# Optimization experiments

Hardware: AMD Instinct MI355X
Metric: run time of the kernel (lower is better)

The kernel has to match this reference:

```python
import jax, jax.numpy as jnp
import numpy as np


def _segsum(x):
    """Stable segment sum: exp(segsum(A)) is 1-semiseparable. x: (..., T) -> (..., T, T)."""
    T = x.shape[-1]
    xx = jnp.broadcast_to(x[..., None], (*x.shape, T))
    xx = jnp.where(jnp.tril(jnp.ones((T, T), bool), -1), xx, 0.0)
    s = jnp.cumsum(xx, axis=-2)
    return jnp.where(jnp.tril(jnp.ones((T, T), bool), 0), s, -jnp.inf)


def setup_inputs() -> dict:
    key = jax.random.key(0)
    ks = jax.random.split(key, 6)
    b, T, h, p, n = 2, 1024, 32, 64, 128
    x = jax.random.normal(ks[0], (b, T, h, p), jnp.float32)
    # negative decay rates, as produced by -exp(A_log)*softplus(dt) in Mamba2
    A = -jax.random.uniform(ks[1], (b, T, h), jnp.float32, minval=0.01, maxval=0.5)
    B = jax.random.normal(ks[2], (b, T, h, n), jnp.float32)
    C = jax.random.normal(ks[3], (b, T, h, n), jnp.float32)
    # retrieval similarity mask (lower-triangular, like segment_and_cosine_similarity output)
    L_mask = jax.random.uniform(ks[4], (b, h, T, T), jnp.float32) * jnp.tril(jnp.ones((T, T), jnp.float32))
    mask_scaling_factor = jnp.float32(0.5)
    return {"x": x, "A": A, "B": B, "C": C, "L_mask": L_mask,
            "mask_scaling_factor": mask_scaling_factor, "chunk_size": 64}


def reference(x, A, B, C, L_mask, mask_scaling_factor, chunk_size):
    b, T, h, p = x.shape
    n = B.shape[-1]
    l = chunk_size
    k = T // l
    # chunk: b (c l) ... -> b c l ...
    xr = x.reshape(b, k, l, h, p)
    Br = B.reshape(b, k, l, h, n)
    Cr = C.reshape(b, k, l, h, n)
    Ar = jnp.transpose(A.reshape(b, k, l, h), (0, 3, 1, 2))  # b h c l
    A_cs = jnp.cumsum(Ar, axis=-1)                            # b h c l
    L = jnp.exp(_segsum(Ar))                                  # b h c l l
    # decompose_diagonal_and_lower_tri(L_mask, chunk_size)
    r = L_mask.reshape(b, h, k, l, k, l)
    didx = np.arange(k)
    L_mask_diag = jnp.moveaxis(r[:, :, didx, :, didx, :], 0, 2)          # b h k l l
    row_idx, col_idx = np.tril_indices(k, -1)                             # strict lower block pairs
    lower_tri = jnp.moveaxis(r[:, :, row_idx, :, col_idx, :], 0, 2)       # b h P l l
    L = L + mask_scaling_factor * L_mask_diag
    # diagonal (intra-chunk) blocks
    Y_diag = jnp.einsum('bclhn,bcshn,bhcls,bcshp->bclhp', Cr, Br, L, xr)
    # retrieval off-diagonal blocks, scatter-added back per destination chunk
    Y_tmp = jnp.einsum('bclhn,bcshn,bhcls,bcshp->bclhp',
                       Cr[:, row_idx], Br[:, col_idx],
                       mask_scaling_factor * lower_tri, xr[:, col_idx])   # b P l h p
    Y_retr = jnp.moveaxis(
        jax.ops.segment_sum(jnp.moveaxis(Y_tmp, 1, 0), jnp.asarray(row_idx), num_segments=k),
        0, 1)                                                             # b k l h p
    # inter-chunk state passing
    decay_states = jnp.exp(A_cs[..., -1:] - A_cs)                         # b h c l
    states = jnp.einsum('bclhn,bhcl,bclhp->bchpn', Br, decay_states, xr)  # b c h p n
    states = jnp.concatenate([jnp.zeros_like(states[:, :1]), states], axis=1)
    decay_chunk = jnp.exp(_segsum(jnp.pad(A_cs[..., -1], ((0, 0), (0, 0), (1, 0)))))  # b h (k+1) (k+1)
    new_states = jnp.einsum('bhzc,bchpn->bzhpn', decay_chunk, states)
    states_in, final_state = new_states[:, :-1], new_states[:, -1]
    Y_off = jnp.einsum('bclhn,bchpn,bhcl->bclhp', Cr, states_in, jnp.exp(A_cs))
    Y = (Y_diag + Y_off + Y_retr).reshape(b, T, h, p)
    return Y, final_state
```

## Files before the change

kernel.cpp:

```cpp
#include <hip/hip_runtime.h>

#define T_ 1024
#define H_ 32
#define P_ 64
#define N_ 128
#define L_ 64

typedef float f32x4 __attribute__((ext_vector_type(4)));
typedef short short8 __attribute__((ext_vector_type(8)));
typedef short short4v __attribute__((ext_vector_type(4)));

static __device__ __forceinline__ unsigned short f2bf(float f) {
  unsigned int u = __float_as_uint(f);
  u += 0x7fffu + ((u >> 16) & 1u);
  return (unsigned short)(u >> 16);
}
static __device__ __forceinline__ float bf2f(short s) {
  return __uint_as_float(((unsigned int)(unsigned short)s) << 16);
}

__global__ __launch_bounds__(1024) void cuma_kernel(const float* __restrict__ A,
                                                    float* __restrict__ cumA) {
  const int bh = blockIdx.x;
  const int b = bh >> 5, h = bh & 31;
  const int t = threadIdx.x;
  __shared__ float s[1024];
  s[t] = A[(b * T_ + t) * H_ + h];
  __syncthreads();
  for (int off = 1; off < 1024; off <<= 1) {
    float v = (t >= off) ? s[t - off] : 0.0f;
    __syncthreads();
    s[t] += v;
    __syncthreads();
  }
  cumA[bh * T_ + t] = s[t];
}

__global__ __launch_bounds__(256) void prep_kernel(
    const float* __restrict__ x, const float* __restrict__ Bm,
    const float* __restrict__ Cm, short* __restrict__ Bbf,
    short* __restrict__ BT, short* __restrict__ Cbf,
    short* __restrict__ xT) {
  const int bh = blockIdx.x;
  const int tb = blockIdx.y;
  const int b = bh >> 5, h = bh & 31;
  const int tid = threadIdx.x;
  __shared__ short Bt[128][72];
  __shared__ short Xt[64][72];

#pragma unroll
  for (int i = 0; i < 8; ++i) {
    const int idx = tid + 256 * i;
    const int row = idx >> 5, n4 = idx & 31;
    const float4 v = *(const float4*)(Bm + ((size_t)(b * T_ + tb * 64 + row) * H_ + h) * N_ + n4 * 4);
    short4v o;
    o.x = (short)f2bf(v.x); o.y = (short)f2bf(v.y);
    o.z = (short)f2bf(v.z); o.w = (short)f2bf(v.w);
    *(short4v*)(Bbf + ((size_t)bh * T_ + tb * 64 + row) * N_ + n4 * 4) = o;
    Bt[n4 * 4 + 0][row] = o.x; Bt[n4 * 4 + 1][row] = o.y;
    Bt[n4 * 4 + 2][row] = o.z; Bt[n4 * 4 + 3][row] = o.w;
  }
#pragma unroll
  for (int i = 0; i < 8; ++i) {
    const int idx = tid + 256 * i;
    const int row = idx >> 5, n4 = idx & 31;
    const float4 v = *(const float4*)(Cm + ((size_t)(b * T_ + tb * 64 + row) * H_ + h) * N_ + n4 * 4);
    short4v o;
    o.x = (short)f2bf(v.x); o.y = (short)f2bf(v.y);
    o.z = (short)f2bf(v.z); o.w = (short)f2bf(v.w);
    *(short4v*)(Cbf + ((size_t)bh * T_ + tb * 64 + row) * N_ + n4 * 4) = o;
  }
#pragma unroll
  for (int i = 0; i < 4; ++i) {
    const int idx = tid + 256 * i;
    const int row = idx >> 4, p4 = idx & 15;
    const float4 v = *(const float4*)(x + ((size_t)(b * T_ + tb * 64 + row) * H_ + h) * P_ + p4 * 4);
    Xt[p4 * 4 + 0][row] = (short)f2bf(v.x);
    Xt[p4 * 4 + 1][row] = (short)f2bf(v.y);
    Xt[p4 * 4 + 2][row] = (short)f2bf(v.z);
    Xt[p4 * 4 + 3][row] = (short)f2bf(v.w);
  }
  __syncthreads();
#pragma unroll
  for (int i = 0; i < 4; ++i) {
    const int idx = tid + 256 * i;
    const int n = idx >> 3, t8 = idx & 7;
    const short4v a = *(const short4v*)&Bt[n][t8 * 8];
    const short4v c = *(const short4v*)&Bt[n][t8 * 8 + 4];
    short8 o;
    o[0] = a.x; o[1] = a.y; o[2] = a.z; o[3] = a.w;
    o[4] = c.x; o[5] = c.y; o[6] = c.z; o[7] = c.w;
    *(short8*)(BT + ((size_t)bh * N_ + n) * T_ + tb * 64 + t8 * 8) = o;
  }
#pragma unroll
  for (int i = 0; i < 2; ++i) {
    const int idx = tid + 256 * i;
    const int p = idx >> 3, t8 = idx & 7;
    const short4v a = *(const short4v*)&Xt[p][t8 * 8];
    const short4v c = *(const short4v*)&Xt[p][t8 * 8 + 4];
    short8 o;
    o[0] = a.x; o[1] = a.y; o[2] = a.z; o[3] = a.w;
    o[4] = c.x; o[5] = c.y; o[6] = c.z; o[7] = c.w;
    *(short8*)(xT + ((size_t)bh * P_ + p) * T_ + tb * 64 + t8 * 8) = o;
  }
}

__global__ __launch_bounds__(256, 2) void attn_kernel(
    const short* __restrict__ xT, const short* __restrict__ Bbf,
    const short* __restrict__ Cbf, const float* __restrict__ mask,
    const float* __restrict__ msf_p, const float* __restrict__ cumA,
    float* __restrict__ Y) {
  const int blk = blockIdx.x;
  const int qc = 15 - (blk >> 6);
  const int bh = blk & 63;
  const int b = bh >> 5, h = bh & 31;
  const float msf = msf_p[0];
  const int tid = threadIdx.x;
  const int w = tid >> 6;
  const int lane = tid & 63;
  const int q = lane >> 4, c = lane & 15;

  __shared__ short Ps[4][16][72];

  short8 cf[4];
  {
    const short* Cg = Cbf + ((size_t)bh * T_ + qc * L_ + 16 * w + c) * N_ + 8 * q;
#pragma unroll
    for (int kt = 0; kt < 4; ++kt) cf[kt] = *(const short8*)(Cg + kt * 32);
  }
  float ca_i[4];
#pragma unroll
  for (int r = 0; r < 4; ++r)
    ca_i[r] = cumA[bh * T_ + qc * L_ + 16 * w + 4 * q + r];

  f32x4 yacc[4];
#pragma unroll
  for (int pt = 0; pt < 4; ++pt) yacc[pt] = (f32x4){0.f, 0.f, 0.f, 0.f};

  const float* mrow0 = mask + ((size_t)bh * T_ + (size_t)(qc * L_ + 16 * w + 4 * q)) * T_ + c;
  const short* Bg0 = Bbf + (size_t)bh * T_ * N_ + 8 * q;
  const short* xg0 = xT + (size_t)bh * P_ * T_ + 8 * q;

  float mvA[16], mvB[16], ckA[4], ckB[4];
#pragma unroll
  for (int tj = 0; tj < 4; ++tj)
#pragma unroll
    for (int r = 0; r < 4; ++r)
      mvA[tj * 4 + r] = __builtin_nontemporal_load(mrow0 + (size_t)r * T_ + 16 * tj);
#pragma unroll
  for (int tj = 0; tj < 4; ++tj) ckA[tj] = cumA[bh * T_ + 16 * tj + c];

#define ATTN_STEP(KC, MVI, CKI, MVO, CKO)                                      \
  {                                                                            \
    const int kc_ = (KC);                                                      \
    const int kcn_ = (kc_ + 1 <= qc) ? (kc_ + 1) : qc;                         \
    short8 bfr[16];                                                            \
    const short* Bg = Bg0 + (size_t)kc_ * L_ * N_;                             \
    _Pragma("unroll") for (int kt = 0; kt < 4; ++kt)                           \
        _Pragma("unroll") for (int tj = 0; tj < 4; ++tj)                       \
            bfr[kt * 4 + tj] =                                                 \
        *(const short8*)(Bg + (size_t)(16 * tj + c) * N_ + kt * 32);           \
    short8 xfr[8];                                                             \
    const short* xg = xg0 + kc_ * L_;                                          \
    _Pragma("unroll") for (int kt2 = 0; kt2 < 2; ++kt2)                        \
        _Pragma("unroll") for (int pt = 0; pt < 4; ++pt)                       \
            xfr[kt2 * 4 + pt] =                                                \
        *(const short8*)(xg + (size_t)(16 * pt + c) * T_ + kt2 * 32);          \
    const float* mb = mrow0 + (size_t)kcn_ * L_;                               \
    _Pragma("unroll") for (int tj = 0; tj < 4; ++tj)                           \
        _Pragma("unroll") for (int r = 0; r < 4; ++r)                          \
            MVO[tj * 4 + r] =                                                  \
        __builtin_nontemporal_load(mb + (size_t)r * T_ + 16 * tj);             \
    _Pragma("unroll") for (int tj = 0; tj < 4; ++tj)                           \
        CKO[tj] = cumA[bh * T_ + kcn_ * L_ + 16 * tj + c];                     \
    f32x4 sacc[4];                                                             \
    _Pragma("unroll") for (int tj = 0; tj < 4; ++tj)                           \
        sacc[tj] = (f32x4){0.f, 0.f, 0.f, 0.f};                                \
    _Pragma("unroll") for (int kt = 0; kt < 4; ++kt)                           \
        _Pragma("unroll") for (int tj = 0; tj < 4; ++tj)                       \
            sacc[tj] = __builtin_amdgcn_mfma_f32_16x16x32_bf16(                \
        cf[kt], bfr[kt * 4 + tj], sacc[tj], 0, 0, 0);                          \
    const bool diag = (kc_ == qc);                                             \
    _Pragma("unroll") for (int tj = 0; tj < 4; ++tj) {                         \
      const int j_l = 16 * tj + c;                                             \
      _Pragma("unroll") for (int r = 0; r < 4; ++r) {                          \
        const int i_l = 16 * w + 4 * q + r;                                    \
        float wgt = __expf(ca_i[r] - CKI[tj]) + msf * MVI[tj * 4 + r];         \
        if (diag && j_l > i_l) wgt = 0.0f;                                     \
        Ps[w][4 * q + r][j_l] = (short)f2bf(sacc[tj][r] * wgt);                \
      }                                                                        \
    }                                                                          \
    _Pragma("unroll") for (int kt2 = 0; kt2 < 2; ++kt2) {                      \
      const short8 pf = *(const short8*)&Ps[w][c][kt2 * 32 + 8 * q];           \
      _Pragma("unroll") for (int pt = 0; pt < 4; ++pt)                         \
          yacc[pt] = __builtin_amdgcn_mfma_f32_16x16x32_bf16(                  \
          pf, xfr[kt2 * 4 + pt], yacc[pt], 0, 0, 0);                           \
    }                                                                          \
  }

  int kc = 0;
  for (; kc + 1 <= qc; kc += 2) {
    ATTN_STEP(kc, mvA, ckA, mvB, ckB)
    ATTN_STEP(kc + 1, mvB, ckB, mvA, ckA)
  }
  if (kc <= qc) {
    ATTN_STEP(kc, mvA, ckA, mvB, ckB)
  }
#undef ATTN_STEP

  float* Yg = Y + ((size_t)(b * T_ + qc * L_ + 16 * w + 4 * q) * H_ + h) * P_;
#pragma unroll
  for (int pt = 0; pt < 4; ++pt)
#pragma unroll
    for (int r = 0; r < 4; ++r)
      __builtin_nontemporal_store(yacc[pt][r], Yg + (size_t)r * (H_ * P_) + 16 * pt + c);
}

__global__ __launch_bounds__(256) void zero_fs(float* __restrict__ fs) {
  const int i = blockIdx.x * 256 + threadIdx.x;
  ((float4*)fs)[i] = make_float4(0.f, 0.f, 0.f, 0.f);
}

__global__ __launch_bounds__(256) void state_kernel(
    const short* __restrict__ xT, const short* __restrict__ BT,
    const float* __restrict__ cumA, float* __restrict__ out) {
  const int bh = blockIdx.x;
  const int tq = blockIdx.y;
  const int tid = threadIdx.x;
  const int w = tid >> 6;
  const int lane = tid & 63;
  const int q = lane >> 4, c = lane & 15;

  __shared__ float wsh[256];
  {
    const float cend = cumA[bh * T_ + (T_ - 1)];
    wsh[tid] = __expf(cend - cumA[bh * T_ + tq * 256 + tid]);
  }
  __syncthreads();

  f32x4 acc[8];
#pragma unroll
  for (int nt = 0; nt < 8; ++nt) acc[nt] = (f32x4){0.f, 0.f, 0.f, 0.f};

#pragma unroll
  for (int ktl = 0; ktl < 8; ++ktl) {
    const int t0 = ktl * 32;
    const int tg = tq * 256 + t0;
    const short8 xv = *(const short8*)(xT + ((size_t)bh * P_ + 16 * w + c) * T_ + tg + 8 * q);
    const float4 w0 = *(const float4*)&wsh[t0 + 8 * q];
    const float4 w1 = *(const float4*)&wsh[t0 + 8 * q + 4];
    short8 af;
    af[0] = (short)f2bf(bf2f(xv[0]) * w0.x); af[1] = (short)f2bf(bf2f(xv[1]) * w0.y);
    af[2] = (short)f2bf(bf2f(xv[2]) * w0.z); af[3] = (short)f2bf(bf2f(xv[3]) * w0.w);
    af[4] = (short)f2bf(bf2f(xv[4]) * w1.x); af[5] = (short)f2bf(bf2f(xv[5]) * w1.y);
    af[6] = (short)f2bf(bf2f(xv[6]) * w1.z); af[7] = (short)f2bf(bf2f(xv[7]) * w1.w);
#pragma unroll
    for (int nt = 0; nt < 8; ++nt) {
      const short8 bf = *(const short8*)(BT + ((size_t)bh * N_ + 16 * nt + c) * T_ + tg + 8 * q);
      acc[nt] = __builtin_amdgcn_mfma_f32_16x16x32_bf16(af, bf, acc[nt], 0, 0, 0);
    }
  }

  float* o = out + (size_t)bh * P_ * N_;
#pragma unroll
  for (int nt = 0; nt < 8; ++nt)
#pragma unroll
    for (int r = 0; r < 4; ++r)
      atomicAdd(&o[(size_t)(16 * w + 4 * q + r) * N_ + 16 * nt + c], acc[nt][r]);
}

extern "C" void kernel_launch(void* const* d_in, const int* in_sizes, int n_in,
                              void* d_out, int out_size, void* d_ws, size_t ws_size,
                              hipStream_t stream) {
  const float* x    = (const float*)d_in[0];
  const float* A    = (const float*)d_in[1];
  const float* Bm   = (const float*)d_in[2];
  const float* Cm   = (const float*)d_in[3];
  const float* mask = (const float*)d_in[4];
  const float* msf  = (const float*)d_in[5];
  float* Y  = (float*)d_out;
  float* fs = (float*)d_out + (size_t)2 * T_ * H_ * P_;

  char* ws = (char*)d_ws;
  float* cumA = (float*)ws;
  size_t off = 1 << 18;
  short* Bbf = (short*)(ws + off); off += (size_t)64 * T_ * N_ * 2;
  short* BT  = (short*)(ws + off); off += (size_t)64 * T_ * N_ * 2;
  short* Cbf = (short*)(ws + off); off += (size_t)64 * T_ * N_ * 2;
  short* xT  = (short*)(ws + off);

  cuma_kernel<<<64, 1024, 0, stream>>>(A, cumA);
  prep_kernel<<<dim3(64, 16), 256, 0, stream>>>(x, Bm, Cm, Bbf, BT, Cbf, xT);
  attn_kernel<<<1024, 256, 0, stream>>>(xT, Bbf, Cbf, mask, msf, cumA, Y);
  zero_fs<<<512, 256, 0, stream>>>(fs);
  state_kernel<<<dim3(64, 4), 256, 0, stream>>>(xT, BT, cumA, fs);
}
```

Before: 506.0 us.

## Pair complementary query chunks per block and use packed bf16 converts with exp2

```diff
diff --git a/kernel.cpp b/kernel.cpp
--- a/kernel.cpp
+++ b/kernel.cpp
@@ -9,14 +9,27 @@
 typedef float f32x4 __attribute__((ext_vector_type(4)));
 typedef short short8 __attribute__((ext_vector_type(8)));
 typedef short short4v __attribute__((ext_vector_type(4)));
-
-static __device__ __forceinline__ unsigned short f2bf(float f) {
-  unsigned int u = __float_as_uint(f);
-  u += 0x7fffu + ((u >> 16) & 1u);
-  return (unsigned short)(u >> 16);
-}
+typedef unsigned int uint2v __attribute__((ext_vector_type(2)));
+typedef unsigned int uint4v __attribute__((ext_vector_type(4)));
+
+#define LOG2E 1.4426950408889634f
+
 static __device__ __forceinline__ float bf2f(short s) {
   return __uint_as_float(((unsigned int)(unsigned short)s) << 16);
+}
+
+static __device__ __forceinline__ unsigned cvt_pk_bf16(float lo, float hi) {
+  unsigned r;
+  asm("v_cvt_pk_bf16_f32 %0, %1, %2" : "=v"(r) : "v"(lo), "v"(hi));
+  return r;
+}
+
+static __device__ __forceinline__ float fexp2(float x) {
+#if __has_builtin(__builtin_amdgcn_exp2f)
+  return __builtin_amdgcn_exp2f(x);
+#else
+  return __expf(x * 0.6931471805599453f);
+#endif
 }
 
 __global__ __launch_bounds__(1024) void cuma_kernel(const float* __restrict__ A,
@@ -33,7 +46,7 @@
     s[t] += v;
     __syncthreads();
   }
-  cumA[bh * T_ + t] = s[t];
+  cumA[bh * T_ + t] = s[t] * LOG2E;
 }
 
 __global__ __launch_bounds__(256) void prep_kernel(
@@ -53,32 +66,32 @@
     const int idx = tid + 256 * i;
     const int row = idx >> 5, n4 = idx & 31;
     const float4 v = *(const float4*)(Bm + ((size_t)(b * T_ + tb * 64 + row) * H_ + h) * N_ + n4 * 4);
-    short4v o;
-    o.x = (short)f2bf(v.x); o.y = (short)f2bf(v.y);
-    o.z = (short)f2bf(v.z); o.w = (short)f2bf(v.w);
-    *(short4v*)(Bbf + ((size_t)bh * T_ + tb * 64 + row) * N_ + n4 * 4) = o;
-    Bt[n4 * 4 + 0][row] = o.x; Bt[n4 * 4 + 1][row] = o.y;
-    Bt[n4 * 4 + 2][row] = o.z; Bt[n4 * 4 + 3][row] = o.w;
+    const unsigned p0 = cvt_pk_bf16(v.x, v.y);
+    const unsigned p1 = cvt_pk_bf16(v.z, v.w);
+    uint2v o; o.x = p0; o.y = p1;
+    *(uint2v*)(Bbf + ((size_t)bh * T_ + tb * 64 + row) * N_ + n4 * 4) = o;
+    Bt[n4 * 4 + 0][row] = (short)p0; Bt[n4 * 4 + 1][row] = (short)(p0 >> 16);
+    Bt[n4 * 4 + 2][row] = (short)p1; Bt[n4 * 4 + 3][row] = (short)(p1 >> 16);
   }
 #pragma unroll
   for (int i = 0; i < 8; ++i) {
     const int idx = tid + 256 * i;
     const int row = idx >> 5, n4 = idx & 31;
     const float4 v = *(const float4*)(Cm + ((size_t)(b * T_ + tb * 64 + row) * H_ + h) * N_ + n4 * 4);
-    short4v o;
-    o.x = (short)f2bf(v.x); o.y = (short)f2bf(v.y);
-    o.z = (short)f2bf(v.z); o.w = (short)f2bf(v.w);
-    *(short4v*)(Cbf + ((size_t)bh * T_ + tb * 64 + row) * N_ + n4 * 4) = o;
+    uint2v o; o.x = cvt_pk_bf16(v.x, v.y); o.y = cvt_pk_bf16(v.z, v.w);
+    *(uint2v*)(Cbf + ((size_t)bh * T_ + tb * 64 + row) * N_ + n4 * 4) = o;
   }
 #pragma unroll
   for (int i = 0; i < 4; ++i) {
     const int idx = tid + 256 * i;
     const int row = idx >> 4, p4 = idx & 15;
     const float4 v = *(const float4*)(x + ((size_t)(b * T_ + tb * 64 + row) * H_ + h) * P_ + p4 * 4);
-    Xt[p4 * 4 + 0][row] = (short)f2bf(v.x);
-    Xt[p4 * 4 + 1][row] = (short)f2bf(v.y);
-    Xt[p4 * 4 + 2][row] = (short)f2bf(v.z);
-    Xt[p4 * 4 + 3][row] = (short)f2bf(v.w);
+    const unsigned p0 = cvt_pk_bf16(v.x, v.y);
+    const unsigned p1 = cvt_pk_bf16(v.z, v.w);
+    Xt[p4 * 4 + 0][row] = (short)p0;
+    Xt[p4 * 4 + 1][row] = (short)(p0 >> 16);
+    Xt[p4 * 4 + 2][row] = (short)p1;
+    Xt[p4 * 4 + 3][row] = (short)(p1 >> 16);
   }
   __syncthreads();
 #pragma unroll
@@ -111,8 +124,8 @@
     const float* __restrict__ msf_p, const float* __restrict__ cumA,
     float* __restrict__ Y) {
   const int blk = blockIdx.x;
-  const int qc = 15 - (blk >> 6);
   const int bh = blk & 63;
+  const int jj = blk >> 6;
   const int b = bh >> 5, h = bh & 31;
   const float msf = msf_p[0];
   const int tid = threadIdx.x;
@@ -122,33 +135,38 @@
 
   __shared__ short Ps[4][16][72];
 
-  short8 cf[4];
-  {
-    const short* Cg = Cbf + ((size_t)bh * T_ + qc * L_ + 16 * w + c) * N_ + 8 * q;
-#pragma unroll
-    for (int kt = 0; kt < 4; ++kt) cf[kt] = *(const short8*)(Cg + kt * 32);
-  }
-  float ca_i[4];
-#pragma unroll
-  for (int r = 0; r < 4; ++r)
-    ca_i[r] = cumA[bh * T_ + qc * L_ + 16 * w + 4 * q + r];
-
-  f32x4 yacc[4];
-#pragma unroll
-  for (int pt = 0; pt < 4; ++pt) yacc[pt] = (f32x4){0.f, 0.f, 0.f, 0.f};
-
-  const float* mrow0 = mask + ((size_t)bh * T_ + (size_t)(qc * L_ + 16 * w + 4 * q)) * T_ + c;
   const short* Bg0 = Bbf + (size_t)bh * T_ * N_ + 8 * q;
   const short* xg0 = xT + (size_t)bh * P_ * T_ + 8 * q;
 
-  float mvA[16], mvB[16], ckA[4], ckB[4];
-#pragma unroll
-  for (int tj = 0; tj < 4; ++tj)
+#pragma unroll 1
+  for (int pass = 0; pass < 2; ++pass) {
+    const int qc = pass ? jj : (15 - jj);
+
+    short8 cf[4];
+    {
+      const short* Cg = Cbf + ((size_t)bh * T_ + qc * L_ + 16 * w + c) * N_ + 8 * q;
+#pragma unroll
+      for (int kt = 0; kt < 4; ++kt) cf[kt] = *(const short8*)(Cg + kt * 32);
+    }
+    float ca_i[4];
 #pragma unroll
     for (int r = 0; r < 4; ++r)
-      mvA[tj * 4 + r] = __builtin_nontemporal_load(mrow0 + (size_t)r * T_ + 16 * tj);
-#pragma unroll
-  for (int tj = 0; tj < 4; ++tj) ckA[tj] = cumA[bh * T_ + 16 * tj + c];
+      ca_i[r] = cumA[bh * T_ + qc * L_ + 16 * w + 4 * q + r];
+
+    f32x4 yacc[4];
+#pragma unroll
+    for (int pt = 0; pt < 4; ++pt) yacc[pt] = (f32x4){0.f, 0.f, 0.f, 0.f};
+
+    const float* mrow0 = mask + ((size_t)bh * T_ + (size_t)(qc * L_ + 16 * w + 4 * q)) * T_ + c;
+
+    float mvA[16], mvB[16], ckA[4], ckB[4];
+#pragma unroll
+    for (int tj = 0; tj < 4; ++tj)
+#pragma unroll
+      for (int r = 0; r < 4; ++r)
+        mvA[tj * 4 + r] = __builtin_nontemporal_load(mrow0 + (size_t)r * T_ + 16 * tj);
+#pragma unroll
+    for (int tj = 0; tj < 4; ++tj) ckA[tj] = cumA[bh * T_ + 16 * tj + c];
 
 #define ATTN_STEP(KC, MVI, CKI, MVO, CKO)                                      \
   {                                                                            \
@@ -183,12 +201,19 @@
     const bool diag = (kc_ == qc);                                             \
     _Pragma("unroll") for (int tj = 0; tj < 4; ++tj) {                         \
       const int j_l = 16 * tj + c;                                             \
+      float fv[4];                                                             \
       _Pragma("unroll") for (int r = 0; r < 4; ++r) {                          \
         const int i_l = 16 * w + 4 * q + r;                                    \
-        float wgt = __expf(ca_i[r] - CKI[tj]) + msf * MVI[tj * 4 + r];         \
+        float wgt = fexp2(ca_i[r] - CKI[tj]) + msf * MVI[tj * 4 + r];          \
         if (diag && j_l > i_l) wgt = 0.0f;                                     \
-        Ps[w][4 * q + r][j_l] = (short)f2bf(sacc[tj][r] * wgt);                \
+        fv[r] = sacc[tj][r] * wgt;                                             \
       }                                                                        \
+      const unsigned p0 = cvt_pk_bf16(fv[0], fv[1]);                           \
+      const unsigned p1 = cvt_pk_bf16(fv[2], fv[3]);                           \
+      Ps[w][4 * q + 0][j_l] = (short)p0;                                       \
+      Ps[w][4 * q + 1][j_l] = (short)(p0 >> 16);                               \
+      Ps[w][4 * q + 2][j_l] = (short)p1;                                       \
+      Ps[w][4 * q + 3][j_l] = (short)(p1 >> 16);                               \
     }                                                                          \
     _Pragma("unroll") for (int kt2 = 0; kt2 < 2; ++kt2) {                      \
       const short8 pf = *(const short8*)&Ps[w][c][kt2 * 32 + 8 * q];           \
@@ -198,22 +223,23 @@
     }                                                                          \
   }
 
-  int kc = 0;
-  for (; kc + 1 <= qc; kc += 2) {
-    ATTN_STEP(kc, mvA, ckA, mvB, ckB)
-    ATTN_STEP(kc + 1, mvB, ckB, mvA, ckA)
-  }
-  if (kc <= qc) {
-    ATTN_STEP(kc, mvA, ckA, mvB, ckB)
-  }
+    int kc = 0;
+    for (; kc + 1 <= qc; kc += 2) {
+      ATTN_STEP(kc, mvA, ckA, mvB, ckB)
+      ATTN_STEP(kc + 1, mvB, ckB, mvA, ckA)
+    }
+    if (kc <= qc) {
+      ATTN_STEP(kc, mvA, ckA, mvB, ckB)
+    }
 #undef ATTN_STEP
 
-  float* Yg = Y + ((size_t)(b * T_ + qc * L_ + 16 * w + 4 * q) * H_ + h) * P_;
-#pragma unroll
-  for (int pt = 0; pt < 4; ++pt)
-#pragma unroll
-    for (int r = 0; r < 4; ++r)
-      __builtin_nontemporal_store(yacc[pt][r], Yg + (size_t)r * (H_ * P_) + 16 * pt + c);
+    float* Yg = Y + ((size_t)(b * T_ + qc * L_ + 16 * w + 4 * q) * H_ + h) * P_;
+#pragma unroll
+    for (int pt = 0; pt < 4; ++pt)
+#pragma unroll
+      for (int r = 0; r < 4; ++r)
+        __builtin_nontemporal_store(yacc[pt][r], Yg + (size_t)r * (H_ * P_) + 16 * pt + c);
+  }
 }
 
 __global__ __launch_bounds__(256) void zero_fs(float* __restrict__ fs) {
@@ -234,7 +260,7 @@
   __shared__ float wsh[256];
   {
     const float cend = cumA[bh * T_ + (T_ - 1)];
-    wsh[tid] = __expf(cend - cumA[bh * T_ + tq * 256 + tid]);
+    wsh[tid] = fexp2(cend - cumA[bh * T_ + tq * 256 + tid]);
   }
   __syncthreads();
 
@@ -249,11 +275,14 @@
     const short8 xv = *(const short8*)(xT + ((size_t)bh * P_ + 16 * w + c) * T_ + tg + 8 * q);
     const float4 w0 = *(const float4*)&wsh[t0 + 8 * q];
     const float4 w1 = *(const float4*)&wsh[t0 + 8 * q + 4];
-    short8 af;
-    af[0] = (short)f2bf(bf2f(xv[0]) * w0.x); af[1] = (short)f2bf(bf2f(xv[1]) * w0.y);
-    af[2] = (short)f2bf(bf2f(xv[2]) * w0.z); af[3] = (short)f2bf(bf2f(xv[3]) * w0.w);
-    af[4] = (short)f2bf(bf2f(xv[4]) * w1.x); af[5] = (short)f2bf(bf2f(xv[5]) * w1.y);
-    af[6] = (short)f2bf(bf2f(xv[6]) * w1.z); af[7] = (short)f2bf(bf2f(xv[7]) * w1.w);
+    const float a0 = bf2f(xv[0]) * w0.x, a1 = bf2f(xv[1]) * w0.y;
+    const float a2 = bf2f(xv[2]) * w0.z, a3 = bf2f(xv[3]) * w0.w;
+    const float a4 = bf2f(xv[4]) * w1.x, a5 = bf2f(xv[5]) * w1.y;
+    const float a6 = bf2f(xv[6]) * w1.z, a7 = bf2f(xv[7]) * w1.w;
+    uint4v uu;
+    uu.x = cvt_pk_bf16(a0, a1); uu.y = cvt_pk_bf16(a2, a3);
+    uu.z = cvt_pk_bf16(a4, a5); uu.w = cvt_pk_bf16(a6, a7);
+    const short8 af = __builtin_bit_cast(short8, uu);
 #pragma unroll
     for (int nt = 0; nt < 8; ++nt) {
       const short8 bf = *(const short8*)(BT + ((size_t)bh * N_ + 16 * nt + c) * T_ + tg + 8 * q);
@@ -291,7 +320,7 @@
 
   cuma_kernel<<<64, 1024, 0, stream>>>(A, cumA);
   prep_kernel<<<dim3(64, 16), 256, 0, stream>>>(x, Bm, Cm, Bbf, BT, Cbf, xT);
-  attn_kernel<<<1024, 256, 0, stream>>>(xT, Bbf, Cbf, mask, msf, cumA, Y);
+  attn_kernel<<<512, 256, 0, stream>>>(xT, Bbf, Cbf, mask, msf, cumA, Y);
   zero_fs<<<512, 256, 0, stream>>>(fs);
   state_kernel<<<dim3(64, 4), 256, 0, stream>>>(xT, BT, cumA, fs);
 }
```

After: 499.8 us. Within noise of the previous version (-1.2%).
